# Performance work log

Hardware: AMD Instinct MI355X
Metric: run time of the kernel (lower is better)

Reference implementation:

```python
import jax, jax.numpy as jnp
import numpy as np

B, L1, L2 = 4, 512, 512
K1D, K2D, V1D, V2D, A = 256, 256, 256, 256, 128


def setup_inputs() -> dict:
    key = jax.random.key(0)
    ks = jax.random.split(key, 12)
    n = lambda i, shape, sc=1.0: (jax.random.normal(ks[i], shape, jnp.float32) * sc)
    return {
        "k1": n(0, (B, L1, K1D)),
        "k2": n(1, (B, L2, K2D)),
        "v1": n(2, (B, L1, V1D)),
        "v2": n(3, (B, L2, V2D)),
        "W1": n(4, (K1D, A), 0.05),
        "b1": n(5, (A,), 0.05),
        "W2": n(6, (K2D, A), 0.05),
        "b2": n(7, (A,), 0.05),
        "ws": n(8, (A,), 0.05),
        "bs": n(9, (), 0.05),
        # lengths in [L/2, L) so every softmax row has at least one finite entry
        "k1_lengths": jax.random.randint(ks[10], (B,), L1 // 2, L1, dtype=jnp.int32),
        "k2_lengths": jax.random.randint(ks[11], (B,), L2 // 2, L2, dtype=jnp.int32),
    }


def reference(k1, k2, v1, v2, W1, b1, W2, b2, ws, bs, k1_lengths, k2_lengths):
    # projected keys: [B,L1,A], [B,L2,A]
    p1 = jnp.einsum("bik,ka->bia", k1, W1) + b1
    p2 = jnp.einsum("bjk,ka->bja", k2, W2) + b2
    h = jnp.tanh(p1[:, :, None, :] + p2[:, None, :, :])  # [B,L1,L2,A]
    score = jnp.einsum("bija,a->bij", h, ws) + bs
    # torch mask semantics: +1 for padded k1 rows, +1 for padded k2 cols, mask where sum == 1
    row_pad = (jnp.arange(L1)[None, :] >= k1_lengths[:, None]).astype(jnp.int32)  # [B,L1]
    col_pad = (jnp.arange(L2)[None, :] >= k2_lengths[:, None]).astype(jnp.int32)  # [B,L2]
    mask = (row_pad[:, :, None] + col_pad[:, None, :]) == 1  # [B,L1,L2]
    score = jnp.where(mask, -jnp.inf, score)
    w1 = jax.nn.softmax(jnp.transpose(score, (0, 2, 1)), axis=-1)  # [B,L2,L1], softmax over L1
    w2 = jax.nn.softmax(score, axis=-1)                             # [B,L1,L2], softmax over L2
    o1 = jnp.matmul(w1, v1)  # [B,L2,V1D]
    o2 = jnp.matmul(w2, v2)  # [B,L1,V2D]
    return (o1, o2, w1, w2, score)
```

## Files before the change

kernel.cpp:

```cpp
#include <hip/hip_runtime.h>
#include <math.h>

#define NB 4
#define NL1 512
#define NL2 512
#define NKD 256
#define NA 128
#define NV 256

#define O1_OFF 0
#define O2_OFF (NB*NL2*NV)
#define W1_OFF (O2_OFF + NB*NL1*NV)
#define W2_OFF (W1_OFF + NB*NL2*NL1)
#define SC_OFF (W2_OFF + NB*NL1*NL2)

#define MASK_NEG (-1e30f)

#define SC2LOG2E 2.8853900817779268f

#if __has_builtin(__builtin_amdgcn_exp2f)
#define EXP2F(x) __builtin_amdgcn_exp2f(x)
#else
#define EXP2F(x) __expf((x) * 0.6931471805599453f)
#endif
#if __has_builtin(__builtin_amdgcn_rcpf)
#define RCPF(x) __builtin_amdgcn_rcpf(x)
#else
#define RCPF(x) (1.0f / (x))
#endif

__global__ __launch_bounds__(128) void proj_kernel(
    const float* __restrict__ k1, const float* __restrict__ k2,
    const float* __restrict__ W1, const float* __restrict__ b1,
    const float* __restrict__ W2, const float* __restrict__ b2,
    float* __restrict__ p1, float* __restrict__ p2)
{
    __shared__ float kr[4][NKD];
    int blk = blockIdx.x;
    int tid = threadIdx.x;
    const float *K, *W, *bias; float* P; int rowbase;
    if (blk < (NB*NL1)/4) { K = k1; W = W1; bias = b1; P = p1; rowbase = blk*4; }
    else                  { K = k2; W = W2; bias = b2; P = p2; rowbase = (blk - (NB*NL1)/4)*4; }
    for (int idx = tid; idx < 256; idx += 128) {
        int r = idx >> 6, c = idx & 63;
        *(float4*)&kr[r][c*4] = *(const float4*)&K[(rowbase + r)*NKD + c*4];
    }
    __syncthreads();
    int a = tid;
    float acc0 = bias[a], acc1 = bias[a], acc2 = bias[a], acc3 = bias[a];
    #pragma unroll 4
    for (int k = 0; k < NKD; k++) {
        float wv = W[k*NA + a];
        acc0 = fmaf(kr[0][k], wv, acc0);
        acc1 = fmaf(kr[1][k], wv, acc1);
        acc2 = fmaf(kr[2][k], wv, acc2);
        acc3 = fmaf(kr[3][k], wv, acc3);
    }
    float s0 = fminf(fmaxf(acc0 * SC2LOG2E, -50.f), 50.f);
    float s1 = fminf(fmaxf(acc1 * SC2LOG2E, -50.f), 50.f);
    float s2 = fminf(fmaxf(acc2 * SC2LOG2E, -50.f), 50.f);
    float s3 = fminf(fmaxf(acc3 * SC2LOG2E, -50.f), 50.f);
    P[(rowbase+0)*NA + a] = EXP2F(s0);
    P[(rowbase+1)*NA + a] = EXP2F(s1);
    P[(rowbase+2)*NA + a] = EXP2F(s2);
    P[(rowbase+3)*NA + a] = EXP2F(s3);
}

#define P1_STRIDE 132
#define P2_STRIDE 68

__global__ __launch_bounds__(256) void score_kernel(
    const float* __restrict__ p1, const float* __restrict__ p2,
    const float* __restrict__ ws, const float* __restrict__ bs,
    const int* __restrict__ len1, const int* __restrict__ len2,
    float* __restrict__ score, float* __restrict__ w1pre)
{
    __shared__ float p1t[64][P1_STRIDE];
    __shared__ float p2t[NA][P2_STRIDE];
    __shared__ float wst[NA];
    __shared__ float wsum[2];
    int b  = blockIdx.z;
    int i0 = blockIdx.y * 64, j0 = blockIdx.x * 64;
    int tid = threadIdx.x;
    if (tid < 128) {
        float w = ws[tid];
        wst[tid] = -2.0f * w;
        float v = w;
        #pragma unroll
        for (int o = 32; o > 0; o >>= 1) v += __shfl_xor(v, o);
        if ((tid & 63) == 0) wsum[tid >> 6] = v;
    }
    const float* p1src = p1 + (b*NL1 + i0)*NA;
    const float* p2src = p2 + (b*NL2 + j0)*NA;
    for (int idx = tid; idx < 2048; idx += 256) {
        int r = idx >> 5, c = idx & 31;
        *(float4*)&p1t[r][c*4] = *(const float4*)&p1src[r*NA + c*4];
    }
    for (int idx = tid; idx < 2048; idx += 256) {
        int j = idx >> 5, c = idx & 31;
        float4 t = *(const float4*)&p2src[j*NA + c*4];
        p2t[c*4+0][j] = t.x; p2t[c*4+1][j] = t.y;
        p2t[c*4+2][j] = t.z; p2t[c*4+3][j] = t.w;
    }
    __syncthreads();

    int tx = tid & 15, ty = tid >> 4;
    int il = ty*4, jl = tx*4;
    float acc[4][4] = {};
    #pragma unroll 2
    for (int a = 0; a < NA; a += 4) {
        float4 wv = *(float4*)&wst[a];
        float4 x0 = *(float4*)&p1t[il  ][a];
        float4 x1 = *(float4*)&p1t[il+1][a];
        float4 x2 = *(float4*)&p1t[il+2][a];
        float4 x3 = *(float4*)&p1t[il+3][a];
        float4 y0 = *(float4*)&p2t[a  ][jl];
        float4 y1 = *(float4*)&p2t[a+1][jl];
        float4 y2 = *(float4*)&p2t[a+2][jl];
        float4 y3 = *(float4*)&p2t[a+3][jl];
        #define TRM(r,c,xq,yq,wq) acc[r][c] = fmaf(wq, RCPF(fmaf(xq, yq, 1.0f)), acc[r][c])
        #define QROW(q, yv, wq) \
            TRM(0,0, x0.q, yv.x, wq); TRM(0,1, x0.q, yv.y, wq); TRM(0,2, x0.q, yv.z, wq); TRM(0,3, x0.q, yv.w, wq); \
            TRM(1,0, x1.q, yv.x, wq); TRM(1,1, x1.q, yv.y, wq); TRM(1,2, x1.q, yv.z, wq); TRM(1,3, x1.q, yv.w, wq); \
            TRM(2,0, x2.q, yv.x, wq); TRM(2,1, x2.q, yv.y, wq); TRM(2,2, x2.q, yv.z, wq); TRM(2,3, x2.q, yv.w, wq); \
            TRM(3,0, x3.q, yv.x, wq); TRM(3,1, x3.q, yv.y, wq); TRM(3,2, x3.q, yv.z, wq); TRM(3,3, x3.q, yv.w, wq)
        QROW(x, y0, wv.x);
        QROW(y, y1, wv.y);
        QROW(z, y2, wv.z);
        QROW(w, y3, wv.w);
        #undef QROW
        #undef TRM
    }
    float sb = wsum[0] + wsum[1] + bs[0];
    int n1 = len1[b], n2 = len2[b];
    float mv[4][4];
    #pragma unroll
    for (int di = 0; di < 4; di++) {
        int gi = i0 + il + di;
        int rp = (gi >= n1);
        #pragma unroll
        for (int dj = 0; dj < 4; dj++) {
            int gj = j0 + jl + dj;
            float val = acc[di][dj] + sb;
            int cp = (gj >= n2);
            if (rp + cp == 1) val = MASK_NEG;
            mv[di][dj] = val;
        }
    }
    #pragma unroll
    for (int di = 0; di < 4; di++) {
        float4 v = make_float4(mv[di][0], mv[di][1], mv[di][2], mv[di][3]);
        *(float4*)&score[(size_t)(b*NL1 + i0 + il + di)*NL2 + j0 + jl] = v;
    }
    #pragma unroll
    for (int dj = 0; dj < 4; dj++) {
        float4 v = make_float4(mv[0][dj], mv[1][dj], mv[2][dj], mv[3][dj]);
        *(float4*)&w1pre[((size_t)b*NL2 + j0 + jl + dj)*NL1 + i0 + il] = v;
    }
}

__global__ __launch_bounds__(256) void softmax_both(const float* __restrict__ score,
                                                    float* __restrict__ w2,
                                                    float* __restrict__ w1)
{
    int row = blockIdx.x * 4 + (threadIdx.x >> 6);
    int lane = threadIdx.x & 63;
    const float* s; float* d;
    if (row < NB*NL1) { s = score + (size_t)row * NL2; d = w2 + (size_t)row * NL2; }
    else { size_t r = row - NB*NL1; s = w1 + r * NL1; d = w1 + r * NL1; }
    float4 v0 = *(const float4*)&s[lane * 4];
    float4 v1 = *(const float4*)&s[256 + lane * 4];
    float m = fmaxf(fmaxf(fmaxf(v0.x, v0.y), fmaxf(v0.z, v0.w)),
                    fmaxf(fmaxf(v1.x, v1.y), fmaxf(v1.z, v1.w)));
    #pragma unroll
    for (int o = 32; o > 0; o >>= 1) m = fmaxf(m, __shfl_xor(m, o));
    float4 e0, e1;
    e0.x = __expf(v0.x - m); e0.y = __expf(v0.y - m);
    e0.z = __expf(v0.z - m); e0.w = __expf(v0.w - m);
    e1.x = __expf(v1.x - m); e1.y = __expf(v1.y - m);
    e1.z = __expf(v1.z - m); e1.w = __expf(v1.w - m);
    float sum = (e0.x + e0.y) + (e0.z + e0.w) + (e1.x + e1.y) + (e1.z + e1.w);
    #pragma unroll
    for (int o = 32; o > 0; o >>= 1) sum += __shfl_xor(sum, o);
    float inv = 1.0f / sum;
    e0.x *= inv; e0.y *= inv; e0.z *= inv; e0.w *= inv;
    e1.x *= inv; e1.y *= inv; e1.z *= inv; e1.w *= inv;
    *(float4*)&d[lane * 4] = e0;
    *(float4*)&d[256 + lane * 4] = e1;
}

typedef __attribute__((ext_vector_type(8))) short bf16x8;
typedef __attribute__((ext_vector_type(4))) float f32x4;

__device__ __forceinline__ unsigned short f2bf(float f) {
    unsigned u = __float_as_uint(f);
    u += 0x7fffu + ((u >> 16) & 1u);
    return (unsigned short)(u >> 16);
}
__device__ __forceinline__ unsigned pk2bf(float a, float b) {
    return (unsigned)f2bf(a) | ((unsigned)f2bf(b) << 16);
}

#define KT 264

__global__ __launch_bounds__(512) void out_matmul(
    const float* __restrict__ w2m, const float* __restrict__ w1m,
    const float* __restrict__ v2,  const float* __restrict__ v1,
    float* __restrict__ o2, float* __restrict__ o1)
{
    __shared__ unsigned short Wt[64 * KT];
    __shared__ unsigned short Vt[64 * KT];
    int z = blockIdx.z; int b = z >> 1, m = z & 1;
    const float* Wm = (m ? w1m : w2m) + (size_t)b * NL1 * NL2;
    const float* Vm = (m ? v1 : v2)   + (size_t)b * NL2 * NV;
    float*       Om = (m ? o1 : o2)   + (size_t)b * NL1 * NV;
    int r0 = blockIdx.y * 64, d0 = blockIdx.x * 64;
    int tid = threadIdx.x;
    int lane = tid & 63, wid = tid >> 6;
    int ry = wid & 3, cx = wid >> 2;
    int lm = lane & 15, kg = lane >> 4;

    const unsigned short* Wf  = &Wt[(ry * 16 + lm) * KT];
    const unsigned short* Vlo = &Vt[(cx * 32 + lm) * KT];
    const unsigned short* Vhi = Vlo + 16 * KT;

    f32x4 acc0 = {0.f,0.f,0.f,0.f}, acc1 = {0.f,0.f,0.f,0.f};

    for (int h = 0; h < 2; h++) {
        if (h) __syncthreads();
        int sbase = h * 256;
        {
            int wr = tid >> 3, wc = tid & 7;
            const float* src = Wm + (size_t)(r0 + wr) * 512 + sbase + wc * 32;
            unsigned short* dst = &Wt[wr * KT + wc * 32];
            #pragma unroll
            for (int k = 0; k < 8; k++) {
                float4 f = *(const float4*)&src[k * 4];
                *(unsigned*)&dst[k * 4]     = pk2bf(f.x, f.y);
                *(unsigned*)&dst[k * 4 + 2] = pk2bf(f.z, f.w);
            }
        }
        {
            int tm = tid & 15, tg = tid >> 4;
            #pragma unroll
            for (int u = 0; u < 4; u++) {
                int s = 2 * tg + 64 * u;
                #pragma unroll
                for (int j = 0; j < 4; j++) {
                    int d = tm + 16 * j;
                    float f0 = Vm[(size_t)(sbase + s) * NV + d0 + d];
                    float f1 = Vm[(size_t)(sbase + s + 1) * NV + d0 + d];
                    *(unsigned*)&Vt[d * KT + s] = pk2bf(f0, f1);
                }
            }
        }
        __syncthreads();
        #pragma unroll 4
        for (int t = 0; t < 8; t++) {
            int s0 = t * 32 + 8 * kg;
            bf16x8 fa  = *(const bf16x8*)(Wf  + s0);
            bf16x8 fb0 = *(const bf16x8*)(Vlo + s0);
            bf16x8 fb1 = *(const bf16x8*)(Vhi + s0);
            acc0 = __builtin_amdgcn_mfma_f32_16x16x32_bf16(fa, fb0, acc0, 0, 0, 0);
            acc1 = __builtin_amdgcn_mfma_f32_16x16x32_bf16(fa, fb1, acc1, 0, 0, 0);
        }
    }

    int rlo = r0 + ry * 16 + 4 * kg;
    int clo = d0 + cx * 32 + lm;
    #pragma unroll
    for (int e = 0; e < 4; e++) {
        Om[(size_t)(rlo + e) * NV + clo]      = acc0[e];
        Om[(size_t)(rlo + e) * NV + clo + 16] = acc1[e];
    }
}

extern "C" void kernel_launch(void* const* d_in, const int* in_sizes, int n_in,
                              void* d_out, int out_size, void* d_ws, size_t ws_size,
                              hipStream_t stream) {
    const float* k1  = (const float*)d_in[0];
    const float* k2  = (const float*)d_in[1];
    const float* v1  = (const float*)d_in[2];
    const float* v2  = (const float*)d_in[3];
    const float* W1  = (const float*)d_in[4];
    const float* b1  = (const float*)d_in[5];
    const float* W2  = (const float*)d_in[6];
    const float* b2  = (const float*)d_in[7];
    const float* wsv = (const float*)d_in[8];
    const float* bsp = (const float*)d_in[9];
    const int* len1  = (const int*)d_in[10];
    const int* len2  = (const int*)d_in[11];

    float* out   = (float*)d_out;
    float* o1    = out + O1_OFF;
    float* o2    = out + O2_OFF;
    float* w1    = out + W1_OFF;
    float* w2    = out + W2_OFF;
    float* score = out + SC_OFF;

    float* p1    = (float*)d_ws;
    float* p2    = p1 + NB*NL2*NA;

    proj_kernel<<<dim3((NB*NL1)/4 + (NB*NL2)/4), 128, 0, stream>>>(k1, k2, W1, b1, W2, b2, p1, p2);
    score_kernel<<<dim3(NL2/64, NL1/64, NB), 256, 0, stream>>>(p1, p2, wsv, bsp, len1, len2, score, w1);
    softmax_both<<<dim3((NB*NL1 + NB*NL2)/4), 256, 0, stream>>>(score, w2, w1);
    out_matmul<<<dim3(NV/64, NL1/64, NB*2), 512, 0, stream>>>(w2, w1, v2, v1, o2, o1);
}
```

Baseline: 62.86 us.

## Pre-convert softmax weights and transposed V to bf16 in earlier kernels

The softmax kernel now also writes bf16 copies of w1/w2 to workspace. The projection kernel gains extra blocks that transpose v1/v2 into a bf16 [d][s] layout. The output matmul then loads ready bf16 tiles with wide vector loads instead of reading fp32, converting, and doing strided transposing loads. This cuts matmul global traffic and uncoalesced V access, at the cost of extra bf16 writes in softmax and more workspace.

```diff
diff --git a/kernel.cpp b/kernel.cpp
--- a/kernel.cpp
+++ b/kernel.cpp
@@ -29,15 +29,53 @@
 #define RCPF(x) (1.0f / (x))
 #endif
 
+__device__ __forceinline__ unsigned short f2bf(float f) {
+    unsigned u = __float_as_uint(f);
+    u += 0x7fffu + ((u >> 16) & 1u);
+    return (unsigned short)(u >> 16);
+}
+__device__ __forceinline__ unsigned pk2bf(float a, float b) {
+    return (unsigned)f2bf(a) | ((unsigned)f2bf(b) << 16);
+}
+
 __global__ __launch_bounds__(128) void proj_kernel(
     const float* __restrict__ k1, const float* __restrict__ k2,
     const float* __restrict__ W1, const float* __restrict__ b1,
     const float* __restrict__ W2, const float* __restrict__ b2,
-    float* __restrict__ p1, float* __restrict__ p2)
+    const float* __restrict__ v1, const float* __restrict__ v2,
+    float* __restrict__ p1, float* __restrict__ p2,
+    unsigned* __restrict__ v1t, unsigned* __restrict__ v2t)
 {
     __shared__ float kr[4][NKD];
+    __shared__ float trbuf[32][68];
     int blk = blockIdx.x;
     int tid = threadIdx.x;
+    if (blk >= 1024) {
+        int idx = blk - 1024;
+        int t = idx >> 8;
+        int rem = idx & 255;
+        int b = rem >> 6;
+        int rem2 = rem & 63;
+        int d0 = (rem2 >> 4) * 64;
+        int s0 = (rem2 & 15) * 32;
+        const float* Vsrc = (t ? v2 : v1) + (size_t)b * NL2 * NV;
+        unsigned* Vdst    = (t ? v2t : v1t) + (size_t)b * NV * (NL2/2);
+        #pragma unroll
+        for (int u = 0; u < 4; u++) {
+            int i2 = tid + 128 * u;
+            int r = i2 >> 4, c = i2 & 15;
+            *(float4*)&trbuf[r][c*4] = *(const float4*)&Vsrc[(size_t)(s0 + r) * NV + d0 + c*4];
+        }
+        __syncthreads();
+        #pragma unroll
+        for (int u = 0; u < 8; u++) {
+            int i2 = tid + 128 * u;
+            int dd = i2 >> 4, c = i2 & 15;
+            Vdst[(size_t)(d0 + dd) * (NL2/2) + (s0 >> 1) + c] =
+                pk2bf(trbuf[2*c][dd], trbuf[2*c+1][dd]);
+        }
+        return;
+    }
     const float *K, *W, *bias; float* P; int rowbase;
     if (blk < (NB*NL1)/4) { K = k1; W = W1; bias = b1; P = p1; rowbase = blk*4; }
     else                  { K = k2; W = W2; bias = b2; P = p2; rowbase = (blk - (NB*NL1)/4)*4; }
@@ -161,13 +199,21 @@
 
 __global__ __launch_bounds__(256) void softmax_both(const float* __restrict__ score,
                                                     float* __restrict__ w2,
-                                                    float* __restrict__ w1)
+                                                    float* __restrict__ w1,
+                                                    unsigned* __restrict__ w2bf,
+                                                    unsigned* __restrict__ w1bf)
 {
     int row = blockIdx.x * 4 + (threadIdx.x >> 6);
     int lane = threadIdx.x & 63;
-    const float* s; float* d;
-    if (row < NB*NL1) { s = score + (size_t)row * NL2; d = w2 + (size_t)row * NL2; }
-    else { size_t r = row - NB*NL1; s = w1 + r * NL1; d = w1 + r * NL1; }
+    const float* s; float* d; unsigned* dbf;
+    if (row < NB*NL1) {
+        s = score + (size_t)row * NL2; d = w2 + (size_t)row * NL2;
+        dbf = w2bf + (size_t)row * (NL2/2);
+    } else {
+        size_t r = row - NB*NL1;
+        s = w1 + r * NL1; d = w1 + r * NL1;
+        dbf = w1bf + r * (NL1/2);
+    }
     float4 v0 = *(const float4*)&s[lane * 4];
     float4 v1 = *(const float4*)&s[256 + lane * 4];
     float m = fmaxf(fmaxf(fmaxf(v0.x, v0.y), fmaxf(v0.z, v0.w)),
@@ -187,33 +233,28 @@
     e1.x *= inv; e1.y *= inv; e1.z *= inv; e1.w *= inv;
     *(float4*)&d[lane * 4] = e0;
     *(float4*)&d[256 + lane * 4] = e1;
+    uint2 lo = make_uint2(pk2bf(e0.x, e0.y), pk2bf(e0.z, e0.w));
+    uint2 hi = make_uint2(pk2bf(e1.x, e1.y), pk2bf(e1.z, e1.w));
+    *(uint2*)&dbf[lane * 2] = lo;
+    *(uint2*)&dbf[128 + lane * 2] = hi;
 }
 
 typedef __attribute__((ext_vector_type(8))) short bf16x8;
 typedef __attribute__((ext_vector_type(4))) float f32x4;
 
-__device__ __forceinline__ unsigned short f2bf(float f) {
-    unsigned u = __float_as_uint(f);
-    u += 0x7fffu + ((u >> 16) & 1u);
-    return (unsigned short)(u >> 16);
-}
-__device__ __forceinline__ unsigned pk2bf(float a, float b) {
-    return (unsigned)f2bf(a) | ((unsigned)f2bf(b) << 16);
-}
-
 #define KT 264
 
 __global__ __launch_bounds__(512) void out_matmul(
-    const float* __restrict__ w2m, const float* __restrict__ w1m,
-    const float* __restrict__ v2,  const float* __restrict__ v1,
+    const unsigned* __restrict__ w2bf, const unsigned* __restrict__ w1bf,
+    const unsigned* __restrict__ v2t,  const unsigned* __restrict__ v1t,
     float* __restrict__ o2, float* __restrict__ o1)
 {
     __shared__ unsigned short Wt[64 * KT];
     __shared__ unsigned short Vt[64 * KT];
     int z = blockIdx.z; int b = z >> 1, m = z & 1;
-    const float* Wm = (m ? w1m : w2m) + (size_t)b * NL1 * NL2;
-    const float* Vm = (m ? v1 : v2)   + (size_t)b * NL2 * NV;
-    float*       Om = (m ? o1 : o2)   + (size_t)b * NL1 * NV;
+    const unsigned* Wb = (m ? w1bf : w2bf) + (size_t)b * NL1 * (NL2/2);
+    const unsigned* Vb = (m ? v1t : v2t)   + (size_t)b * NV * (NL2/2);
+    float*          Om = (m ? o1 : o2)     + (size_t)b * NL1 * NV;
     int r0 = blockIdx.y * 64, d0 = blockIdx.x * 64;
     int tid = threadIdx.x;
     int lane = tid & 63, wid = tid >> 6;
@@ -226,33 +267,18 @@
 
     f32x4 acc0 = {0.f,0.f,0.f,0.f}, acc1 = {0.f,0.f,0.f,0.f};
 
+    int wr = tid >> 3, c0 = tid & 7;
     for (int h = 0; h < 2; h++) {
         if (h) __syncthreads();
-        int sbase = h * 256;
-        {
-            int wr = tid >> 3, wc = tid & 7;
-            const float* src = Wm + (size_t)(r0 + wr) * 512 + sbase + wc * 32;
-            unsigned short* dst = &Wt[wr * KT + wc * 32];
-            #pragma unroll
-            for (int k = 0; k < 8; k++) {
-                float4 f = *(const float4*)&src[k * 4];
-                *(unsigned*)&dst[k * 4]     = pk2bf(f.x, f.y);
-                *(unsigned*)&dst[k * 4 + 2] = pk2bf(f.z, f.w);
-            }
-        }
-        {
-            int tm = tid & 15, tg = tid >> 4;
-            #pragma unroll
-            for (int u = 0; u < 4; u++) {
-                int s = 2 * tg + 64 * u;
-                #pragma unroll
-                for (int j = 0; j < 4; j++) {
-                    int d = tm + 16 * j;
-                    float f0 = Vm[(size_t)(sbase + s) * NV + d0 + d];
-                    float f1 = Vm[(size_t)(sbase + s + 1) * NV + d0 + d];
-                    *(unsigned*)&Vt[d * KT + s] = pk2bf(f0, f1);
-                }
-            }
+        const unsigned* srcW = Wb + (size_t)(r0 + wr) * (NL2/2) + h * 128;
+        const unsigned* srcV = Vb + (size_t)(d0 + wr) * (NL2/2) + h * 128;
+        unsigned short* dstW = &Wt[wr * KT];
+        unsigned short* dstV = &Vt[wr * KT];
+        #pragma unroll
+        for (int k = 0; k < 4; k++) {
+            int c = c0 + 8 * k;
+            *(uint4*)&dstW[c * 8] = *(const uint4*)&srcW[c * 4];
+            *(uint4*)&dstV[c * 8] = *(const uint4*)&srcV[c * 4];
         }
         __syncthreads();
         #pragma unroll 4
@@ -298,11 +324,16 @@
     float* w2    = out + W2_OFF;
     float* score = out + SC_OFF;
 
-    float* p1    = (float*)d_ws;
-    float* p2    = p1 + NB*NL2*NA;
-
-    proj_kernel<<<dim3((NB*NL1)/4 + (NB*NL2)/4), 128, 0, stream>>>(k1, k2, W1, b1, W2, b2, p1, p2);
+    float* p1       = (float*)d_ws;
+    float* p2       = p1 + NB*NL1*NA;
+    unsigned* w2bf  = (unsigned*)(p2 + NB*NL2*NA);
+    unsigned* w1bf  = w2bf + (size_t)NB*NL1*(NL2/2);
+    unsigned* v2t   = w1bf + (size_t)NB*NL2*(NL1/2);
+    unsigned* v1t   = v2t + (size_t)NB*NV*(NL2/2);
+
+    proj_kernel<<<dim3((NB*NL1)/4 + (NB*NL2)/4 + 512), 128, 0, stream>>>(
+        k1, k2, W1, b1, W2, b2, v1, v2, p1, p2, v1t, v2t);
     score_kernel<<<dim3(NL2/64, NL1/64, NB), 256, 0, stream>>>(p1, p2, wsv, bsp, len1, len2, score, w1);
-    softmax_both<<<dim3((NB*NL1 + NB*NL2)/4), 256, 0, stream>>>(score, w2, w1);
-    out_matmul<<<dim3(NV/64, NL1/64, NB*2), 512, 0, stream>>>(w2, w1, v2, v1, o2, o1);
-}
+    softmax_both<<<dim3((NB*NL1 + NB*NL2)/4), 256, 0, stream>>>(score, w2, w1, w2bf, w1bf);
+    out_matmul<<<dim3(NV/64, NL1/64, NB*2), 512, 0, stream>>>(w2bf, w1bf, v2t, v1t, o2, o1);
+}
```

Measured after the change: 60.25 us. 1.04x faster.
